# Performance work log

Hardware: AMD Instinct MI355X
Metric: run time of the kernel (lower is better)

The kernel has to match this reference:

```python
import jax, jax.numpy as jnp
import numpy as np

LN_EPS = 1e-5

def _layernorm(x, g, b):
    mu = jnp.mean(x, axis=-1, keepdims=True)
    var = jnp.var(x, axis=-1, keepdims=True)
    return (x - mu) * jax.lax.rsqrt(var + LN_EPS) * g + b

def setup_inputs() -> dict:
    key = jax.random.key(0)
    ks = jax.random.split(key, 12)
    B, E, R = 32, 64, 36
    Dt, Di, D = 768, 2048, 512
    s = 0.02
    return {
        "text_feats": jax.random.normal(ks[0], (B, E, Dt), jnp.float32),
        "image_feats": jax.random.normal(ks[1], (B, R, Di), jnp.float32),
        "W_text": jax.random.normal(ks[2], (Dt, D), jnp.float32) * s,
        "b_text": jnp.zeros((D,), jnp.float32),
        "g_text": jnp.ones((D,), jnp.float32),
        "beta_text": jnp.zeros((D,), jnp.float32),
        "W_img": jax.random.normal(ks[3], (Di, D), jnp.float32) * s,
        "b_img": jnp.zeros((D,), jnp.float32),
        "g_img": jnp.ones((D,), jnp.float32),
        "beta_img": jnp.zeros((D,), jnp.float32),
        "W1": jax.random.normal(ks[4], (2 * D, D), jnp.float32) * s,
        "b1": jnp.zeros((D,), jnp.float32),
        "W2": jax.random.normal(ks[5], (D, 1), jnp.float32) * s,
        "b2": jnp.zeros((1,), jnp.float32),
    }

def reference(text_feats, image_feats, W_text, b_text, g_text, beta_text,
              W_img, b_img, g_img, beta_img, W1, b1, W2, b2):
    B, E, _ = text_feats.shape
    R = image_feats.shape[1]
    D = W_text.shape[1]
    # projections: Linear -> ReLU -> LayerNorm
    text_aligned = _layernorm(jax.nn.relu(text_feats @ W_text + b_text), g_text, beta_text)   # [B,E,D]
    image_aligned = _layernorm(jax.nn.relu(image_feats @ W_img + b_img), g_img, beta_img)     # [B,R,D]
    # pairwise scorer: split W1 to avoid materializing the [B,E,R,2D] concat
    W1_t, W1_i = W1[:D], W1[D:]
    h_t = text_aligned @ W1_t                 # [B,E,D]
    h_i = image_aligned @ W1_i + b1           # [B,R,D]
    h = jax.nn.relu(h_t[:, :, None, :] + h_i[:, None, :, :])  # [B,E,R,D]
    scores_raw = jnp.squeeze(h @ W2, -1) + b2[0]               # [B,E,R]
    alignment_scores = jax.nn.sigmoid(scores_raw)
    # softmax over flattened (E*R) per batch
    w = jax.nn.softmax(alignment_scores.reshape(B, E * R), axis=1).reshape(B, E, R)
    # weighted sum over regions, mean over entities
    aggregated = jnp.einsum('ber,brd->bd', w, image_aligned) / E   # [B,D]
    return alignment_scores, aggregated
```

## Files before the change

kernel.cpp:

```cpp
#include <hip/hip_runtime.h>
#include <math.h>

#define LN_EPS 1e-5f

typedef __attribute__((ext_vector_type(8))) short bf16x8;
typedef __attribute__((ext_vector_type(4))) float f32x4;
typedef unsigned short ushort_t;
typedef unsigned int uint_t;

__device__ __forceinline__ ushort_t f2bf(float f) {
    uint_t u = __float_as_uint(f);
    u += 0x7FFF + ((u >> 16) & 1);
    return (ushort_t)(u >> 16);
}

__device__ __forceinline__ bf16x8 cvt8(float4 a, float4 b) {
    bf16x8 r;
    r[0] = (short)f2bf(a.x); r[1] = (short)f2bf(a.y);
    r[2] = (short)f2bf(a.z); r[3] = (short)f2bf(a.w);
    r[4] = (short)f2bf(b.x); r[5] = (short)f2bf(b.y);
    r[6] = (short)f2bf(b.z); r[7] = (short)f2bf(b.w);
    return r;
}

__global__ __launch_bounds__(256) void prep_kernel(
    const float* __restrict__ W_text, const float* __restrict__ W_img,
    const float* __restrict__ W1,
    ushort_t* __restrict__ Wt_t, ushort_t* __restrict__ Wi_t,
    ushort_t* __restrict__ W1t_t, ushort_t* __restrict__ W1i_t,
    float* __restrict__ stats)
{
    __shared__ float t[32][33];
    int local = blockIdx.x;
    if (local >= 1920) {
        for (int i = threadIdx.x; i < 6400; i += 256) stats[i] = 0.f;
        return;
    }
    const float* src; ushort_t* dst; int K;
    if      (local < 384)  { src = W_text;         dst = Wt_t;  K = 768;  }
    else if (local < 1408) { src = W_img;          dst = Wi_t;  K = 2048; local -= 384; }
    else if (local < 1664) { src = W1;             dst = W1t_t; K = 512;  local -= 1408; }
    else                   { src = W1 + 512 * 512; dst = W1i_t; K = 512;  local -= 1664; }
    const int ntk = K / 32;
    const int k0 = (local % ntk) * 32;
    const int n0 = (local / ntk) * 32;
    const int x = threadIdx.x % 32, y = threadIdx.x / 32;
    #pragma unroll
    for (int j = 0; j < 4; ++j)
        t[y + 8 * j][x] = src[(size_t)(k0 + y + 8 * j) * 512 + n0 + x];
    __syncthreads();
    #pragma unroll
    for (int j = 0; j < 4; ++j)
        dst[(size_t)(n0 + y + 8 * j) * K + k0 + x] = f2bf(t[x][y + 8 * j]);
}

__global__ __launch_bounds__(256) void proj_kernel(
    const float* __restrict__ A0, const ushort_t* __restrict__ B0,
    const float* __restrict__ bias0, float* __restrict__ C0, int K0,
    const float* __restrict__ A1, const ushort_t* __restrict__ B1,
    const float* __restrict__ bias1, float* __restrict__ C1, int K1,
    float* __restrict__ stats, int ysplit)
{
    __shared__ float red[4][64][64];

    const float* A; const ushort_t* Bt; const float* bias; float* C; int K, srow;
    int yy = blockIdx.y;
    if (yy < ysplit) { A = A0; Bt = B0; bias = bias0; C = C0; K = K0; srow = yy * 64; }
    else { A = A1; Bt = B1; bias = bias1; C = C1; K = K1; yy -= ysplit; srow = 2048 + yy * 64; }

    const int tid  = threadIdx.x;
    const int wave = tid >> 6;
    const int lane = tid & 63;
    const int q    = lane >> 4;
    const int mj   = lane & 15;
    const int brow = yy * 64;
    const int bcol = blockIdx.x * 64;

    const float*    Ab = A  + (size_t)(brow + mj) * K + q * 8;
    const ushort_t* Bb = Bt + (size_t)(bcol + mj) * K + q * 8;
    const int kw0    = wave * (K >> 2);
    const int ksteps = K >> 7;

    f32x4 acc[4][4] = {};

    #pragma unroll 2
    for (int s = 0; s < ksteps; ++s) {
        const int k = kw0 + s * 32;
        bf16x8 af[4], bf[4];
        #pragma unroll
        for (int i = 0; i < 4; ++i) {
            const float* pA = Ab + (size_t)i * 16 * K + k;
            float4 x0 = *(const float4*)pA;
            float4 x1 = *(const float4*)(pA + 4);
            af[i] = cvt8(x0, x1);
            bf[i] = *(const bf16x8*)(Bb + (size_t)i * 16 * K + k);
        }
        #pragma unroll
        for (int mi = 0; mi < 4; ++mi)
            #pragma unroll
            for (int ni = 0; ni < 4; ++ni)
                acc[mi][ni] = __builtin_amdgcn_mfma_f32_16x16x32_bf16(
                    af[mi], bf[ni], acc[mi][ni], 0, 0, 0);
    }

    #pragma unroll
    for (int mi = 0; mi < 4; ++mi)
        #pragma unroll
        for (int ni = 0; ni < 4; ++ni)
            #pragma unroll
            for (int r = 0; r < 4; ++r)
                red[wave][mi * 16 + q * 4 + r][ni * 16 + mj] = acc[mi][ni][r];
    __syncthreads();

    #pragma unroll
    for (int g = 0; g < 4; ++g) {
        const int idx = g * 1024 + tid * 4;
        const int row = idx >> 6, col = idx & 63;
        float4 v0 = *(float4*)&red[0][row][col];
        float4 v1 = *(float4*)&red[1][row][col];
        float4 v2 = *(float4*)&red[2][row][col];
        float4 v3 = *(float4*)&red[3][row][col];
        float4 bv = *(const float4*)&bias[bcol + col];
        float4 o;
        o.x = fmaxf((v0.x + v1.x) + (v2.x + v3.x) + bv.x, 0.f);
        o.y = fmaxf((v0.y + v1.y) + (v2.y + v3.y) + bv.y, 0.f);
        o.z = fmaxf((v0.z + v1.z) + (v2.z + v3.z) + bv.z, 0.f);
        o.w = fmaxf((v0.w + v1.w) + (v2.w + v3.w) + bv.w, 0.f);
        *(float4*)&C[(size_t)(brow + row) * 512 + bcol + col] = o;
        float s  = (o.x + o.y) + (o.z + o.w);
        float ss = (o.x * o.x + o.y * o.y) + (o.z * o.z + o.w * o.w);
        #pragma unroll
        for (int m = 1; m < 16; m <<= 1) {
            s  += __shfl_xor(s, m);
            ss += __shfl_xor(ss, m);
        }
        if ((tid & 15) == 0) {
            atomicAdd(&stats[(size_t)(srow + row) * 2], s);
            atomicAdd(&stats[(size_t)(srow + row) * 2 + 1], ss);
        }
    }
}

__global__ __launch_bounds__(256) void h_kernel(
    const float* __restrict__ A0, const ushort_t* __restrict__ B0,
    const float* __restrict__ bias0, float* __restrict__ C0,
    const float* __restrict__ g0, const float* __restrict__ be0, int soff0,
    const float* __restrict__ A1, const ushort_t* __restrict__ B1,
    const float* __restrict__ bias1, float* __restrict__ C1,
    const float* __restrict__ g1, const float* __restrict__ be1, int soff1,
    const float* __restrict__ stats, int ysplit)
{
    __shared__ float red[4][64][64];

    const float* A; const ushort_t* Bt; const float* bias; float* C;
    const float* g; const float* be; int soff;
    int yy = blockIdx.y;
    if (yy < ysplit) { A = A0; Bt = B0; bias = bias0; C = C0; g = g0; be = be0; soff = soff0; }
    else { A = A1; Bt = B1; bias = bias1; C = C1; g = g1; be = be1; soff = soff1; yy -= ysplit; }

    const int tid  = threadIdx.x;
    const int wave = tid >> 6;
    const int lane = tid & 63;
    const int q    = lane >> 4;
    const int mj   = lane & 15;
    const int brow = yy * 64;
    const int bcol = blockIdx.x * 64;

    float mu[4], rstd[4];
    #pragma unroll
    for (int i = 0; i < 4; ++i) {
        const int row = soff + brow + i * 16 + mj;
        float2 st = *(const float2*)&stats[(size_t)row * 2];
        float m   = st.x * (1.f / 512.f);
        float var = st.y * (1.f / 512.f) - m * m;
        mu[i] = m; rstd[i] = rsqrtf(var + LN_EPS);
    }

    const float*    Ab = A  + (size_t)(brow + mj) * 512 + q * 8;
    const ushort_t* Bb = Bt + (size_t)(bcol + mj) * 512 + q * 8;
    const int kw0 = wave * 128;

    f32x4 acc[4][4] = {};

    #pragma unroll 2
    for (int s = 0; s < 4; ++s) {
        const int k = kw0 + s * 32;
        float4 gv0 = *(const float4*)&g[k + q * 8];
        float4 gv1 = *(const float4*)&g[k + q * 8 + 4];
        float4 bv0 = *(const float4*)&be[k + q * 8];
        float4 bv1 = *(const float4*)&be[k + q * 8 + 4];
        bf16x8 af[4], bf[4];
        #pragma unroll
        for (int i = 0; i < 4; ++i) {
            const float* pA = Ab + (size_t)i * 16 * 512 + k;
            float4 x0 = *(const float4*)pA;
            float4 x1 = *(const float4*)(pA + 4);
            float4 t0, t1;
            t0.x = fmaf((x0.x - mu[i]) * rstd[i], gv0.x, bv0.x);
            t0.y = fmaf((x0.y - mu[i]) * rstd[i], gv0.y, bv0.y);
            t0.z = fmaf((x0.z - mu[i]) * rstd[i], gv0.z, bv0.z);
            t0.w = fmaf((x0.w - mu[i]) * rstd[i], gv0.w, bv0.w);
            t1.x = fmaf((x1.x - mu[i]) * rstd[i], gv1.x, bv1.x);
            t1.y = fmaf((x1.y - mu[i]) * rstd[i], gv1.y, bv1.y);
            t1.z = fmaf((x1.z - mu[i]) * rstd[i], gv1.z, bv1.z);
            t1.w = fmaf((x1.w - mu[i]) * rstd[i], gv1.w, bv1.w);
            af[i] = cvt8(t0, t1);
            bf[i] = *(const bf16x8*)(Bb + (size_t)i * 16 * 512 + k);
        }
        #pragma unroll
        for (int mi = 0; mi < 4; ++mi)
            #pragma unroll
            for (int ni = 0; ni < 4; ++ni)
                acc[mi][ni] = __builtin_amdgcn_mfma_f32_16x16x32_bf16(
                    af[mi], bf[ni], acc[mi][ni], 0, 0, 0);
    }

    #pragma unroll
    for (int mi = 0; mi < 4; ++mi)
        #pragma unroll
        for (int ni = 0; ni < 4; ++ni)
            #pragma unroll
            for (int r = 0; r < 4; ++r)
                red[wave][mi * 16 + q * 4 + r][ni * 16 + mj] = acc[mi][ni][r];
    __syncthreads();

    #pragma unroll
    for (int gq = 0; gq < 4; ++gq) {
        const int idx = gq * 1024 + tid * 4;
        const int row = idx >> 6, col = idx & 63;
        float4 v0 = *(float4*)&red[0][row][col];
        float4 v1 = *(float4*)&red[1][row][col];
        float4 v2 = *(float4*)&red[2][row][col];
        float4 v3 = *(float4*)&red[3][row][col];
        float4 o;
        o.x = (v0.x + v1.x) + (v2.x + v3.x);
        o.y = (v0.y + v1.y) + (v2.y + v3.y);
        o.z = (v0.z + v1.z) + (v2.z + v3.z);
        o.w = (v0.w + v1.w) + (v2.w + v3.w);
        if (bias) {
            float4 bv = *(const float4*)&bias[bcol + col];
            o.x += bv.x; o.y += bv.y; o.z += bv.z; o.w += bv.w;
        }
        *(float4*)&C[(size_t)(brow + row) * 512 + bcol + col] = o;
    }
}

__global__ __launch_bounds__(256) void scores_kernel(
    const float* __restrict__ ht, const float* __restrict__ hi,
    const float* __restrict__ W2, const float* __restrict__ b2,
    float* __restrict__ scores)
{
    const int blk  = blockIdx.x;
    const int b    = blk >> 4;
    const int e0   = (blk & 15) * 4;
    const int tid  = threadIdx.x;
    const int lane = tid & 63;
    const int wave = tid >> 6;

    float htv[4][8], w2v[8];
    #pragma unroll
    for (int e = 0; e < 4; ++e) {
        const float* htp = ht + (size_t)(b * 64 + e0 + e) * 512;
        #pragma unroll
        for (int j = 0; j < 8; ++j) htv[e][j] = htp[lane + 64 * j];
    }
    #pragma unroll
    for (int j = 0; j < 8; ++j) w2v[j] = W2[lane + 64 * j];
    const float bb = b2[0];
    const float* hib = hi + (size_t)b * 36 * 512;

    for (int r = wave; r < 36; r += 4) {
        const float* hir = hib + (size_t)r * 512;
        float hv[8];
        #pragma unroll
        for (int j = 0; j < 8; ++j) hv[j] = hir[lane + 64 * j];
        float a0 = 0.f, a1 = 0.f, a2 = 0.f, a3 = 0.f;
        #pragma unroll
        for (int j = 0; j < 8; ++j) {
            a0 = fmaf(fmaxf(htv[0][j] + hv[j], 0.f), w2v[j], a0);
            a1 = fmaf(fmaxf(htv[1][j] + hv[j], 0.f), w2v[j], a1);
            a2 = fmaf(fmaxf(htv[2][j] + hv[j], 0.f), w2v[j], a2);
            a3 = fmaf(fmaxf(htv[3][j] + hv[j], 0.f), w2v[j], a3);
        }
        #pragma unroll
        for (int off = 32; off; off >>= 1) {
            a0 += __shfl_down(a0, off);
            a1 += __shfl_down(a1, off);
            a2 += __shfl_down(a2, off);
            a3 += __shfl_down(a3, off);
        }
        if (lane == 0) {
            float* sp = scores + (size_t)(b * 64 + e0) * 36 + r;
            sp[0]      = 1.f / (1.f + expf(-(a0 + bb)));
            sp[36]     = 1.f / (1.f + expf(-(a1 + bb)));
            sp[72]     = 1.f / (1.f + expf(-(a2 + bb)));
            sp[108]    = 1.f / (1.f + expf(-(a3 + bb)));
        }
    }
}

__global__ __launch_bounds__(256) void agg_kernel(
    const float* __restrict__ scores, const float* __restrict__ ia_raw,
    const float* __restrict__ stats2,
    const float* __restrict__ g, const float* __restrict__ beta,
    float* __restrict__ outAgg)
{
    const int b   = blockIdx.x;
    const int tid = threadIdx.x;
    const float* sc = scores + (size_t)b * 2304;

    __shared__ float part[4][36];
    __shared__ float wsr[36];
    __shared__ float tmp[36];
    __shared__ float inv_s, c1_s;

    const int e4 = tid >> 6;
    const int r  = tid & 63;
    if (r < 36) {
        float p = 0.f;
        #pragma unroll
        for (int e = 0; e < 16; ++e) p += expf(sc[(e * 4 + e4) * 36 + r]);
        part[e4][r] = p;
    }
    __syncthreads();
    if (tid < 36) wsr[tid] = part[0][tid] + part[1][tid] + part[2][tid] + part[3][tid];
    __syncthreads();
    if (tid < 64) {
        float v = (tid < 36) ? wsr[tid] : 0.f;
        #pragma unroll
        for (int off = 32; off; off >>= 1) v += __shfl_down(v, off);
        if (tid == 0) inv_s = 1.f / (v * 64.f);
    }
    __syncthreads();
    if (tid < 36) {
        const int row = b * 36 + tid;
        float2 st = *(const float2*)&stats2[(size_t)row * 2];
        float m   = st.x * (1.f / 512.f);
        float var = st.y * (1.f / 512.f) - m * m;
        float rs  = rsqrtf(var + LN_EPS);
        float W   = wsr[tid] * inv_s;
        wsr[tid]  = W * rs;
        tmp[tid]  = W * rs * m;
    }
    __syncthreads();
    if (tid < 64) {
        float v = (tid < 36) ? tmp[tid] : 0.f;
        #pragma unroll
        for (int off = 32; off; off >>= 1) v += __shfl_down(v, off);
        if (tid == 0) c1_s = v;
    }
    __syncthreads();
    const float c1 = c1_s;

    const float* ib = ia_raw + (size_t)b * 36 * 512;
    for (int d = tid; d < 512; d += 256) {
        float acc = 0.f;
        #pragma unroll
        for (int rr = 0; rr < 36; ++rr)
            acc = fmaf(wsr[rr], ib[rr * 512 + d], acc);
        outAgg[(size_t)b * 512 + d] = g[d] * (acc - c1) + beta[d] * (1.f / 64.f);
    }
}

extern "C" void kernel_launch(void* const* d_in, const int* in_sizes, int n_in,
                              void* d_out, int out_size, void* d_ws, size_t ws_size,
                              hipStream_t stream)
{
    const float* text      = (const float*)d_in[0];
    const float* image     = (const float*)d_in[1];
    const float* W_text    = (const float*)d_in[2];
    const float* b_text    = (const float*)d_in[3];
    const float* g_text    = (const float*)d_in[4];
    const float* beta_text = (const float*)d_in[5];
    const float* W_img     = (const float*)d_in[6];
    const float* b_img     = (const float*)d_in[7];
    const float* g_img     = (const float*)d_in[8];
    const float* beta_img  = (const float*)d_in[9];
    const float* W1        = (const float*)d_in[10];
    const float* b1        = (const float*)d_in[11];
    const float* W2        = (const float*)d_in[12];
    const float* b2        = (const float*)d_in[13];

    float* out_scores = (float*)d_out;
    float* out_agg    = (float*)d_out + 73728;

    char* ws = (char*)d_ws;
    float*    ta    = (float*)(ws);
    float*    ia    = (float*)(ws + 4194304);
    float*    ht    = (float*)(ws + 6553600);
    float*    hi    = (float*)(ws + 10747904);
    ushort_t* Wt_t  = (ushort_t*)(ws + 13107200);
    ushort_t* Wi_t  = (ushort_t*)(ws + 13893632);
    ushort_t* W1t_t = (ushort_t*)(ws + 15990784);
    ushort_t* W1i_t = (ushort_t*)(ws + 16515072);
    float*    stats = (float*)(ws + 17039360);

    prep_kernel<<<1921, 256, 0, stream>>>(W_text, W_img, W1,
                                          Wt_t, Wi_t, W1t_t, W1i_t, stats);
    proj_kernel<<<dim3(8, 50), 256, 0, stream>>>(
        text, Wt_t, b_text, ta, 768,
        image, Wi_t, b_img, ia, 2048,
        stats, 32);
    h_kernel<<<dim3(8, 50), 256, 0, stream>>>(
        ta, W1t_t, nullptr, ht, g_text, beta_text, 0,
        ia, W1i_t, b1, hi, g_img, beta_img, 2048,
        stats, 32);
    scores_kernel<<<512, 256, 0, stream>>>(ht, hi, W2, b2, out_scores);
    agg_kernel<<<32, 256, 0, stream>>>(out_scores, ia, stats + 4096,
                                       g_img, beta_img, out_agg);
}
```

Baseline: 154.3 us.

## Pre-convert activations to bf16 in prep and fuse aggregation into scores kernel

The prep kernel now also converts the text and image activations to bf16 in a separate pass, so the projection GEMM loads bf16 A tiles directly instead of converting fp32 on every load. Each projection block re-reads its A tiles across the 8 column blocks, so the in-loop conversion was repeated work. The scores and aggregation kernels are merged: a per-batch atomic counter picks the last finishing block, which then does the softmax and weighted sum. This removes one kernel launch. The cost is an extra full read and write of the activations in prep, plus threadfence and atomic overhead in the fused kernel.

```diff
diff --git a/kernel.cpp b/kernel.cpp
--- a/kernel.cpp
+++ b/kernel.cpp
@@ -24,18 +24,33 @@
 }
 
 __global__ __launch_bounds__(256) void prep_kernel(
+    const float* __restrict__ text, const float* __restrict__ image,
+    ushort_t* __restrict__ text_bf, ushort_t* __restrict__ image_bf,
     const float* __restrict__ W_text, const float* __restrict__ W_img,
     const float* __restrict__ W1,
     ushort_t* __restrict__ Wt_t, ushort_t* __restrict__ Wi_t,
     ushort_t* __restrict__ W1t_t, ushort_t* __restrict__ W1i_t,
-    float* __restrict__ stats)
+    float* __restrict__ stats, int* __restrict__ counters)
 {
     __shared__ float t[32][33];
-    int local = blockIdx.x;
-    if (local >= 1920) {
+    const int bid = blockIdx.x;
+    if (bid < 3840) {
+        const int i4 = (bid * 256 + threadIdx.x) * 4;
+        const float* src; ushort_t* dst; int off;
+        if (i4 < 1572864) { src = text;  dst = text_bf;  off = i4; }
+        else              { src = image; dst = image_bf; off = i4 - 1572864; }
+        float4 v = *(const float4*)(src + off);
+        ushort4 o;
+        o.x = f2bf(v.x); o.y = f2bf(v.y); o.z = f2bf(v.z); o.w = f2bf(v.w);
+        *(ushort4*)(dst + off) = o;
+        return;
+    }
+    if (bid >= 5760) {
         for (int i = threadIdx.x; i < 6400; i += 256) stats[i] = 0.f;
+        if (threadIdx.x < 32) counters[threadIdx.x] = 0;
         return;
     }
+    int local = bid - 3840;
     const float* src; ushort_t* dst; int K;
     if      (local < 384)  { src = W_text;         dst = Wt_t;  K = 768;  }
     else if (local < 1408) { src = W_img;          dst = Wi_t;  K = 2048; local -= 384; }
@@ -55,15 +70,15 @@
 }
 
 __global__ __launch_bounds__(256) void proj_kernel(
-    const float* __restrict__ A0, const ushort_t* __restrict__ B0,
+    const ushort_t* __restrict__ A0, const ushort_t* __restrict__ B0,
     const float* __restrict__ bias0, float* __restrict__ C0, int K0,
-    const float* __restrict__ A1, const ushort_t* __restrict__ B1,
+    const ushort_t* __restrict__ A1, const ushort_t* __restrict__ B1,
     const float* __restrict__ bias1, float* __restrict__ C1, int K1,
     float* __restrict__ stats, int ysplit)
 {
-    __shared__ float red[4][64][64];
-
-    const float* A; const ushort_t* Bt; const float* bias; float* C; int K, srow;
+    __shared__ __align__(16) float red[4][64][64];
+
+    const ushort_t* A; const ushort_t* Bt; const float* bias; float* C; int K, srow;
     int yy = blockIdx.y;
     if (yy < ysplit) { A = A0; Bt = B0; bias = bias0; C = C0; K = K0; srow = yy * 64; }
     else { A = A1; Bt = B1; bias = bias1; C = C1; K = K1; yy -= ysplit; srow = 2048 + yy * 64; }
@@ -76,7 +91,7 @@
     const int brow = yy * 64;
     const int bcol = blockIdx.x * 64;
 
-    const float*    Ab = A  + (size_t)(brow + mj) * K + q * 8;
+    const ushort_t* Ab = A  + (size_t)(brow + mj) * K + q * 8;
     const ushort_t* Bb = Bt + (size_t)(bcol + mj) * K + q * 8;
     const int kw0    = wave * (K >> 2);
     const int ksteps = K >> 7;
@@ -86,21 +101,18 @@
     #pragma unroll 2
     for (int s = 0; s < ksteps; ++s) {
         const int k = kw0 + s * 32;
-        bf16x8 af[4], bf[4];
+        bf16x8 af[4], bfr[4];
         #pragma unroll
         for (int i = 0; i < 4; ++i) {
-            const float* pA = Ab + (size_t)i * 16 * K + k;
-            float4 x0 = *(const float4*)pA;
-            float4 x1 = *(const float4*)(pA + 4);
-            af[i] = cvt8(x0, x1);
-            bf[i] = *(const bf16x8*)(Bb + (size_t)i * 16 * K + k);
+            af[i]  = *(const bf16x8*)(Ab + (size_t)i * 16 * K + k);
+            bfr[i] = *(const bf16x8*)(Bb + (size_t)i * 16 * K + k);
         }
         #pragma unroll
         for (int mi = 0; mi < 4; ++mi)
             #pragma unroll
             for (int ni = 0; ni < 4; ++ni)
                 acc[mi][ni] = __builtin_amdgcn_mfma_f32_16x16x32_bf16(
-                    af[mi], bf[ni], acc[mi][ni], 0, 0, 0);
+                    af[mi], bfr[ni], acc[mi][ni], 0, 0, 0);
     }
 
     #pragma unroll
@@ -113,8 +125,8 @@
     __syncthreads();
 
     #pragma unroll
-    for (int g = 0; g < 4; ++g) {
-        const int idx = g * 1024 + tid * 4;
+    for (int g4 = 0; g4 < 4; ++g4) {
+        const int idx = g4 * 1024 + tid * 4;
         const int row = idx >> 6, col = idx & 63;
         float4 v0 = *(float4*)&red[0][row][col];
         float4 v1 = *(float4*)&red[1][row][col];
@@ -150,7 +162,7 @@
     const float* __restrict__ g1, const float* __restrict__ be1, int soff1,
     const float* __restrict__ stats, int ysplit)
 {
-    __shared__ float red[4][64][64];
+    __shared__ __align__(16) float red[4][64][64];
 
     const float* A; const ushort_t* Bt; const float* bias; float* C;
     const float* g; const float* be; int soff;
@@ -189,7 +201,7 @@
         float4 gv1 = *(const float4*)&g[k + q * 8 + 4];
         float4 bv0 = *(const float4*)&be[k + q * 8];
         float4 bv1 = *(const float4*)&be[k + q * 8 + 4];
-        bf16x8 af[4], bf[4];
+        bf16x8 af[4], bfr[4];
         #pragma unroll
         for (int i = 0; i < 4; ++i) {
             const float* pA = Ab + (size_t)i * 16 * 512 + k;
@@ -204,15 +216,15 @@
             t1.y = fmaf((x1.y - mu[i]) * rstd[i], gv1.y, bv1.y);
             t1.z = fmaf((x1.z - mu[i]) * rstd[i], gv1.z, bv1.z);
             t1.w = fmaf((x1.w - mu[i]) * rstd[i], gv1.w, bv1.w);
-            af[i] = cvt8(t0, t1);
-            bf[i] = *(const bf16x8*)(Bb + (size_t)i * 16 * 512 + k);
+            af[i]  = cvt8(t0, t1);
+            bfr[i] = *(const bf16x8*)(Bb + (size_t)i * 16 * 512 + k);
         }
         #pragma unroll
         for (int mi = 0; mi < 4; ++mi)
             #pragma unroll
             for (int ni = 0; ni < 4; ++ni)
                 acc[mi][ni] = __builtin_amdgcn_mfma_f32_16x16x32_bf16(
-                    af[mi], bf[ni], acc[mi][ni], 0, 0, 0);
+                    af[mi], bfr[ni], acc[mi][ni], 0, 0, 0);
     }
 
     #pragma unroll
@@ -225,8 +237,8 @@
     __syncthreads();
 
     #pragma unroll
-    for (int gq = 0; gq < 4; ++gq) {
-        const int idx = gq * 1024 + tid * 4;
+    for (int g4 = 0; g4 < 4; ++g4) {
+        const int idx = g4 * 1024 + tid * 4;
         const int row = idx >> 6, col = idx & 63;
         float4 v0 = *(float4*)&red[0][row][col];
         float4 v1 = *(float4*)&red[1][row][col];
@@ -245,14 +257,18 @@
     }
 }
 
-__global__ __launch_bounds__(256) void scores_kernel(
+__global__ __launch_bounds__(256) void scores_agg_kernel(
     const float* __restrict__ ht, const float* __restrict__ hi,
+    const float* __restrict__ ia_raw,
     const float* __restrict__ W2, const float* __restrict__ b2,
-    float* __restrict__ scores)
+    const float* __restrict__ stats2,
+    const float* __restrict__ g, const float* __restrict__ beta,
+    float* __restrict__ out_scores, float* __restrict__ out_agg,
+    int* __restrict__ counters)
 {
-    const int blk  = blockIdx.x;
-    const int b    = blk >> 4;
-    const int e0   = (blk & 15) * 4;
+    const int u    = blockIdx.x;
+    const int b    = u >> 4;
+    const int e0   = (u & 15) * 4;
     const int tid  = threadIdx.x;
     const int lane = tid & 63;
     const int wave = tid >> 6;
@@ -290,29 +306,26 @@
             a3 += __shfl_down(a3, off);
         }
         if (lane == 0) {
-            float* sp = scores + (size_t)(b * 64 + e0) * 36 + r;
-            sp[0]      = 1.f / (1.f + expf(-(a0 + bb)));
-            sp[36]     = 1.f / (1.f + expf(-(a1 + bb)));
-            sp[72]     = 1.f / (1.f + expf(-(a2 + bb)));
-            sp[108]    = 1.f / (1.f + expf(-(a3 + bb)));
-        }
-    }
-}
-
-__global__ __launch_bounds__(256) void agg_kernel(
-    const float* __restrict__ scores, const float* __restrict__ ia_raw,
-    const float* __restrict__ stats2,
-    const float* __restrict__ g, const float* __restrict__ beta,
-    float* __restrict__ outAgg)
-{
-    const int b   = blockIdx.x;
-    const int tid = threadIdx.x;
-    const float* sc = scores + (size_t)b * 2304;
+            float* sp = out_scores + (size_t)(b * 64 + e0) * 36 + r;
+            sp[0]   = 1.f / (1.f + expf(-(a0 + bb)));
+            sp[36]  = 1.f / (1.f + expf(-(a1 + bb)));
+            sp[72]  = 1.f / (1.f + expf(-(a2 + bb)));
+            sp[108] = 1.f / (1.f + expf(-(a3 + bb)));
+        }
+    }
+
+    __threadfence();
+    __shared__ int is_last;
+    if (tid == 0) is_last = (atomicAdd(&counters[b], 1) == 15);
+    __syncthreads();
+    if (!is_last) return;
+    __threadfence();
 
     __shared__ float part[4][36];
     __shared__ float wsr[36];
     __shared__ float tmp[36];
-    __shared__ float inv_s, c1_s;
+    __shared__ float msc[2];
+    const float* sc = out_scores + (size_t)b * 2304;
 
     const int e4 = tid >> 6;
     const int r  = tid & 63;
@@ -329,7 +342,7 @@
         float v = (tid < 36) ? wsr[tid] : 0.f;
         #pragma unroll
         for (int off = 32; off; off >>= 1) v += __shfl_down(v, off);
-        if (tid == 0) inv_s = 1.f / (v * 64.f);
+        if (tid == 0) msc[0] = 1.f / (v * 64.f);
     }
     __syncthreads();
     if (tid < 36) {
@@ -338,7 +351,7 @@
         float m   = st.x * (1.f / 512.f);
         float var = st.y * (1.f / 512.f) - m * m;
         float rs  = rsqrtf(var + LN_EPS);
-        float W   = wsr[tid] * inv_s;
+        float W   = wsr[tid] * msc[0];
         wsr[tid]  = W * rs;
         tmp[tid]  = W * rs * m;
     }
@@ -347,18 +360,17 @@
         float v = (tid < 36) ? tmp[tid] : 0.f;
         #pragma unroll
         for (int off = 32; off; off >>= 1) v += __shfl_down(v, off);
-        if (tid == 0) c1_s = v;
-    }
-    __syncthreads();
-    const float c1 = c1_s;
-
+        if (tid == 0) msc[1] = v;
+    }
+    __syncthreads();
+    const float c1 = msc[1];
     const float* ib = ia_raw + (size_t)b * 36 * 512;
     for (int d = tid; d < 512; d += 256) {
         float acc = 0.f;
         #pragma unroll
         for (int rr = 0; rr < 36; ++rr)
             acc = fmaf(wsr[rr], ib[rr * 512 + d], acc);
-        outAgg[(size_t)b * 512 + d] = g[d] * (acc - c1) + beta[d] * (1.f / 64.f);
+        out_agg[(size_t)b * 512 + d] = g[d] * (acc - c1) + beta[d] * (1.f / 64.f);
     }
 }
 
@@ -385,27 +397,32 @@
     float* out_agg    = (float*)d_out + 73728;
 
     char* ws = (char*)d_ws;
-    float*    ta    = (float*)(ws);
-    float*    ia    = (float*)(ws + 4194304);
-    float*    ht    = (float*)(ws + 6553600);
-    float*    hi    = (float*)(ws + 10747904);
-    ushort_t* Wt_t  = (ushort_t*)(ws + 13107200);
-    ushort_t* Wi_t  = (ushort_t*)(ws + 13893632);
-    ushort_t* W1t_t = (ushort_t*)(ws + 15990784);
-    ushort_t* W1i_t = (ushort_t*)(ws + 16515072);
-    float*    stats = (float*)(ws + 17039360);
-
-    prep_kernel<<<1921, 256, 0, stream>>>(W_text, W_img, W1,
-                                          Wt_t, Wi_t, W1t_t, W1i_t, stats);
+    ushort_t* text_bf  = (ushort_t*)(ws);
+    ushort_t* image_bf = (ushort_t*)(ws + 3145728);
+    float*    ta       = (float*)(ws + 7864320);
+    float*    ia       = (float*)(ws + 12058624);
+    float*    ht       = (float*)(ws + 14417920);
+    float*    hi       = (float*)(ws + 18612224);
+    ushort_t* Wt_t     = (ushort_t*)(ws + 20971520);
+    ushort_t* Wi_t     = (ushort_t*)(ws + 21757952);
+    ushort_t* W1t_t    = (ushort_t*)(ws + 23855104);
+    ushort_t* W1i_t    = (ushort_t*)(ws + 24379392);
+    float*    stats    = (float*)(ws + 24903680);
+    int*      counters = (int*)(ws + 24929280);
+
+    prep_kernel<<<5761, 256, 0, stream>>>(text, image, text_bf, image_bf,
+                                          W_text, W_img, W1,
+                                          Wt_t, Wi_t, W1t_t, W1i_t,
+                                          stats, counters);
     proj_kernel<<<dim3(8, 50), 256, 0, stream>>>(
-        text, Wt_t, b_text, ta, 768,
-        image, Wi_t, b_img, ia, 2048,
+        text_bf, Wt_t, b_text, ta, 768,
+        image_bf, Wi_t, b_img, ia, 2048,
         stats, 32);
     h_kernel<<<dim3(8, 50), 256, 0, stream>>>(
         ta, W1t_t, nullptr, ht, g_text, beta_text, 0,
         ia, W1i_t, b1, hi, g_img, beta_img, 2048,
         stats, 32);
-    scores_kernel<<<512, 256, 0, stream>>>(ht, hi, W2, b2, out_scores);
-    agg_kernel<<<32, 256, 0, stream>>>(out_scores, ia, stats + 4096,
-                                       g_img, beta_img, out_agg);
-}
+    scores_agg_kernel<<<512, 256, 0, stream>>>(
+        ht, hi, ia, W2, b2, stats + 4096, g_img, beta_img,
+        out_scores, out_agg, counters);
+}
```

Result: slower. 190.8 us (+23.7%).
